# Kernel optimization log

Measured on AMD Instinct MI355X. Metric: run time of the kernel, lower is better.

## Reference

```python
import jax, jax.numpy as jnp
import numpy as np

B, T, C = 4, 1024, 768
N_HEAD = 12
HEAD_DIM = C // N_HEAD          # 64
WINDOW = 256                    # sliding window size
FIRE_WIDTH = 32
FIRE_INIT_L = 512.0
FIRE_EPS = 1e-6
ROPE_THETA = 10000.0


def setup_inputs() -> dict:
    key = jax.random.key(0)
    ks = jax.random.split(key, 8)
    s = 0.02
    return {
        "x": jax.random.normal(ks[0], (B, T, C), dtype=jnp.float32),
        "Wq": jax.random.normal(ks[1], (C, C), dtype=jnp.float32) * s,
        "Wk": jax.random.normal(ks[2], (C, C), dtype=jnp.float32) * s,
        "Wv": jax.random.normal(ks[3], (C, C), dtype=jnp.float32) * s,
        "Wproj": jax.random.normal(ks[4], (C, C), dtype=jnp.float32) * s,
        "fire_w1": jax.random.normal(ks[5], (1, FIRE_WIDTH), dtype=jnp.float32) * s,
        "fire_b1": jnp.zeros((FIRE_WIDTH,), dtype=jnp.float32),
        "fire_w2": jax.random.normal(ks[6], (FIRE_WIDTH, N_HEAD), dtype=jnp.float32) * s,
        "fire_b2": jnp.zeros((N_HEAD,), dtype=jnp.float32),
        "fire_c": jnp.asarray(0.1, dtype=jnp.float32),
        "fire_Lmult": jnp.asarray(1.0, dtype=jnp.float32),
        "iter_num": 1000,
    }


def _rope(t):
    # t: [B, H, T, D]; half-split rotary embedding
    d = t.shape[-1]
    pos = jnp.arange(t.shape[2], dtype=t.dtype)
    inv_freq = 1.0 / (ROPE_THETA ** (jnp.arange(0, d, 2, dtype=t.dtype) / d))
    ang = pos[:, None] * inv_freq[None, :]            # [T, D/2]
    cos, sin = jnp.cos(ang), jnp.sin(ang)
    t1, t2 = t[..., : d // 2], t[..., d // 2 :]
    return jnp.concatenate([t1 * cos - t2 * sin, t1 * sin + t2 * cos], axis=-1)


def _fire_bias(w1, b1, w2, b2, c, Lmult, Tlen, dtype):
    # FIRE: psi(i-j)/psi(max(i, L)) -> tiny MLP -> per-head bias [H, T, T]
    pos = jnp.arange(Tlen, dtype=dtype)
    rel = pos[:, None] - pos[None, :]                 # [T, T]
    thresh = jnp.abs(Lmult * FIRE_INIT_L)
    pos_norm = jnp.maximum(pos, thresh)
    rel_log = jnp.log(jnp.abs(c * rel) + 1.0)
    norm_log = jnp.log(jnp.abs(c * pos_norm) + 1.0) + FIRE_EPS
    z = (rel_log / norm_log[:, None])[..., None]      # [T, T, 1]
    h = jax.nn.relu(z @ w1 + b1)                      # [T, T, W]
    bias = h @ w2 + b2                                # [T, T, H]
    return jnp.transpose(bias, (2, 0, 1))             # [H, T, T]


def reference(x, Wq, Wk, Wv, Wproj, fire_w1, fire_b1, fire_w2, fire_b2,
              fire_c, fire_Lmult, iter_num):
    Bx, Tx, Cx = x.shape
    q = (x @ Wq).reshape(Bx, Tx, N_HEAD, HEAD_DIM).transpose(0, 2, 1, 3)
    k = (x @ Wk).reshape(Bx, Tx, N_HEAD, HEAD_DIM).transpose(0, 2, 1, 3)
    v = (x @ Wv).reshape(Bx, Tx, N_HEAD, HEAD_DIM).transpose(0, 2, 1, 3)
    q, k = _rope(q), _rope(k)

    att = jnp.einsum("bhqd,bhkd->bhqk", q, k) / jnp.sqrt(
        jnp.asarray(HEAD_DIM, x.dtype))
    att = att + _fire_bias(fire_w1, fire_b1, fire_w2, fire_b2,
                           fire_c, fire_Lmult, Tx, x.dtype)[None]

    # sliding-window causal mask: 0 <= q_idx - kv_idx <= WINDOW
    idx = jnp.arange(Tx)
    rel = idx[:, None] - idx[None, :]
    allowed = (rel >= 0) & (rel <= WINDOW)            # [T, T]
    att = jnp.where(allowed[None, None], att, jnp.asarray(-jnp.inf, att.dtype))
    att = jax.nn.softmax(att, axis=-1)

    y = jnp.einsum("bhqk,bhkd->bhqd", att, v)
    y = y.transpose(0, 2, 1, 3).reshape(Bx, Tx, Cx)
    return y @ Wproj
```

## Files before the change

### kernel.cpp

```cpp
#include <hip/hip_runtime.h>

typedef unsigned short u16;
typedef __attribute__((ext_vector_type(8))) short bf16x8;
typedef __attribute__((ext_vector_type(4))) float f32x4;

#define NB 4
#define NT 1024
#define NC 768
#define NH 12
#define HD 64

__device__ __forceinline__ u16 f2bf(float f) {
  union { float f; unsigned u; } v; v.f = f;
  unsigned r = v.u + 0x7FFFu + ((v.u >> 16) & 1u);
  return (u16)(r >> 16);
}
__device__ __forceinline__ float bf2f(u16 h) {
  union { unsigned u; float f; } v; v.u = ((unsigned)h) << 16;
  return v.f;
}

__device__ __forceinline__ void gld16(const u16* g, u16* l) {
  __builtin_amdgcn_global_load_lds((const __attribute__((address_space(1))) void*)g,
                                   (__attribute__((address_space(3))) void*)l, 16, 0, 0);
}

__global__ __launch_bounds__(256) void prep_k(const float* __restrict__ x,
                                              const float* __restrict__ Wq,
                                              const float* __restrict__ Wk,
                                              const float* __restrict__ Wv,
                                              const float* __restrict__ Wp,
                                              const float* __restrict__ w1,
                                              const float* __restrict__ b1,
                                              const float* __restrict__ w2,
                                              const float* __restrict__ b2,
                                              const float* __restrict__ cP,
                                              const float* __restrict__ LmP,
                                              u16* __restrict__ xb,
                                              u16* __restrict__ Wt,
                                              u16* __restrict__ Wtp,
                                              u16* __restrict__ ebias) {
  __shared__ u16 tile[64][65];
  const int bid = blockIdx.x;
  const int tid = threadIdx.x;
  if (bid < 1536) {
    const int base = bid * 2048 + tid * 8;
    const f32x4* xv = (const f32x4*)(x + base);
    f32x4 v0 = xv[0], v1 = xv[1];
    bf16x8 o;
#pragma unroll
    for (int j = 0; j < 4; ++j) {
      o[j] = (short)f2bf(v0[j]);
      o[4 + j] = (short)f2bf(v1[j]);
    }
    *(bf16x8*)(xb + base) = o;
  } else if (bid < 2112) {
    int idx = bid - 1536;
    int z = idx / 144, rem = idx - z * 144;
    int k0 = (rem / 12) * 64, n0 = (rem % 12) * 64;
    const float* src = (z == 0) ? Wq : (z == 1) ? Wk : (z == 2) ? Wv : Wp;
    const int c = tid & 63, r4 = tid >> 6;
#pragma unroll
    for (int p = 0; p < 16; ++p) {
      int kk = p * 4 + r4;
      tile[kk][c] = f2bf(src[(size_t)(k0 + kk) * NC + n0 + c]);
    }
    __syncthreads();
    u16* dst = (z < 3) ? (Wt + (size_t)z * NC * NC) : Wtp;
#pragma unroll
    for (int p = 0; p < 16; ++p) {
      int nn = p * 4 + r4;
      dst[(size_t)(n0 + nn) * NC + k0 + c] = tile[c][nn];
    }
  } else {
    int q = bid - 2112;
    float c = cP[0], Lm = LmP[0];
    float thresh = fabsf(Lm * 512.0f);
    float pn = fmaxf((float)q, thresh);
    float inv_nl = 1.0f / (logf(fabsf(c * pn) + 1.0f) + 1e-6f);
    for (int idx = tid; idx < 384; idx += 256) {
      int rel = idx - 64;
      float out[NH];
      if (rel >= 0 && rel <= 256) {
        float z = logf(fabsf(c * (float)rel) + 1.0f) * inv_nl;
        float acc[NH];
#pragma unroll
        for (int hh = 0; hh < NH; ++hh) acc[hh] = b2[hh];
#pragma unroll
        for (int j = 0; j < 32; ++j) {
          float hj = fmaxf(z * w1[j] + b1[j], 0.0f);
#pragma unroll
          for (int hh = 0; hh < NH; ++hh) acc[hh] += hj * w2[j * NH + hh];
        }
#pragma unroll
        for (int hh = 0; hh < NH; ++hh) out[hh] = __expf(acc[hh]);
      } else {
#pragma unroll
        for (int hh = 0; hh < NH; ++hh) out[hh] = 0.0f;
      }
#pragma unroll
      for (int hh = 0; hh < NH; ++hh)
        ebias[((size_t)hh * NT + q) * 384 + idx] = f2bf(out[hh]);
    }
  }
}

__global__ __launch_bounds__(256, 3) void gemm_qkv_rope(const u16* __restrict__ A,
                                                        const u16* __restrict__ Bt,
                                                        u16* __restrict__ Qp,
                                                        u16* __restrict__ Kp,
                                                        u16* __restrict__ Vp) {
  constexpr int K = NC;
  __shared__ __align__(16) u16 smem[9472];
  u16* As = smem;
  u16* Bs = smem + 4096;
  const int tid = threadIdx.x;
  const int wid = tid >> 6, lane = tid & 63;
  const int wr = wid >> 1, wc = wid & 1;
  const int m0 = blockIdx.x * 128, n0 = blockIdx.y * 128;
  const int lr = lane & 15, lg = lane >> 4, lk = lg << 3;
  const int srow = wid * 16 + (lane >> 2);
  const int scol = (lane & 3) * 8;
  f32x4 acc[4][4] = {};
  const u16* Ag = A + (size_t)(m0 + srow) * K + scol;
  const u16* Bg = Bt + (size_t)(n0 + srow) * K + scol;
  u16* Al = &As[(wid * 16) * 32];
  u16* Bl = &Bs[(wid * 16) * 32];

  for (int k0 = 0; k0 < K; k0 += 32) {
    gld16(Ag + k0, Al);
    gld16(Ag + (size_t)64 * K + k0, Al + 64 * 32);
    gld16(Bg + k0, Bl);
    gld16(Bg + (size_t)64 * K + k0, Bl + 64 * 32);
    __syncthreads();
    bf16x8 af[4], bfv[4];
#pragma unroll
    for (int i = 0; i < 4; ++i)
      af[i] = *(const bf16x8*)&As[(wr * 64 + i * 16 + lr) * 32 + lk];
#pragma unroll
    for (int j = 0; j < 4; ++j)
      bfv[j] = *(const bf16x8*)&Bs[(wc * 64 + j * 16 + lr) * 32 + lk];
#pragma unroll
    for (int i = 0; i < 4; ++i)
#pragma unroll
      for (int j = 0; j < 4; ++j)
        acc[i][j] = __builtin_amdgcn_mfma_f32_16x16x32_bf16(af[i], bfv[j], acc[i][j], 0, 0, 0);
    __syncthreads();
  }

  const int rbase = lg * 4;
  const int base_col = n0 + wc * 64;
  const int part = base_col / 768;
  const int h = (base_col % 768) >> 6;
  const int b = m0 >> 10;
  const int bh = b * NH + h;
  const int tbase = (m0 & 1023) + wr * 64;

  if (part < 2) {
    u16* dst = (part == 0 ? Qp : Kp) + ((size_t)bh << 16);
    const float inv0 = __expf(-(float)lr * 0.28782313662425f);
    const float inv1 = __expf(-(float)(lr + 16) * 0.28782313662425f);
#pragma unroll
    for (int i = 0; i < 4; ++i)
#pragma unroll
      for (int rr = 0; rr < 4; ++rr) {
        const int tl = tbase + i * 16 + rbase + rr;
        float s0, c0, s1, c1;
        __sincosf((float)tl * inv0, &s0, &c0);
        __sincosf((float)tl * inv1, &s1, &c1);
        const float a0 = acc[i][0][rr], a1 = acc[i][1][rr];
        const float a2 = acc[i][2][rr], a3 = acc[i][3][rr];
        const size_t ro = (size_t)tl * HD;
        dst[ro + lr]      = f2bf(a0 * c0 - a2 * s0);
        dst[ro + 16 + lr] = f2bf(a1 * c1 - a3 * s1);
        dst[ro + 32 + lr] = f2bf(a0 * s0 + a2 * c0);
        dst[ro + 48 + lr] = f2bf(a1 * s1 + a3 * c1);
      }
  } else {
    u16* dst = Vp + ((size_t)bh << 16);
    u16* vb = smem + wid * 64 * 37;
#pragma unroll
    for (int hf = 0; hf < 2; ++hf) {
#pragma unroll
      for (int i = 0; i < 4; ++i)
#pragma unroll
        for (int rr = 0; rr < 4; ++rr) {
          const int row = i * 16 + rbase + rr;
          vb[row * 37 + lr]      = f2bf(acc[i][2 * hf][rr]);
          vb[row * 37 + 16 + lr] = f2bf(acc[i][2 * hf + 1][rr]);
        }
      asm volatile("s_waitcnt lgkmcnt(0)" ::: "memory");
#pragma unroll
      for (int p = 0; p < 32; ++p) {
        const int d = hf * 32 + p;
        dst[(size_t)d * NT + tbase + lane] = vb[lane * 37 + p];
      }
    }
  }
}

template <bool F32OUT, int WR, int WC, int AI, int BJ>
__global__ __launch_bounds__(256, 4) void gemm_lds(const u16* __restrict__ A,
                                                   const u16* __restrict__ Bt,
                                                   void* __restrict__ Cv,
                                                   int M, int N, int K) {
  constexpr int BM = WR * AI * 16;
  constexpr int BN = WC * BJ * 16;
  __shared__ u16 As[BM * 32];
  __shared__ u16 Bs[BN * 32];
  const int tid = threadIdx.x;
  const int wid = tid >> 6, lane = tid & 63;
  const int wr = wid / WC, wc = wid % WC;
  const int m0 = blockIdx.x * BM, n0 = blockIdx.y * BN;
  const int lr = lane & 15, lk = (lane >> 4) << 3;
  const int srow = wid * 16 + (lane >> 2);
  const int scol = (lane & 3) * 8;
  f32x4 acc[AI][BJ] = {};
  const u16* Ag = A + (size_t)(m0 + srow) * K + scol;
  const u16* Bg = Bt + (size_t)(n0 + srow) * K + scol;
  u16* Al = &As[(wid * 16) * 32];
  u16* Bl = &Bs[(wid * 16) * 32];

  for (int k0 = 0; k0 < K; k0 += 32) {
#pragma unroll
    for (int ia = 0; ia < BM / 64; ++ia)
      gld16(Ag + (size_t)(ia * 64) * K + k0, Al + ia * 64 * 32);
#pragma unroll
    for (int ib = 0; ib < BN / 64; ++ib)
      gld16(Bg + (size_t)(ib * 64) * K + k0, Bl + ib * 64 * 32);
    __syncthreads();
    bf16x8 af[AI], bfv[BJ];
#pragma unroll
    for (int i = 0; i < AI; ++i)
      af[i] = *(const bf16x8*)&As[(wr * AI * 16 + i * 16 + lr) * 32 + lk];
#pragma unroll
    for (int j = 0; j < BJ; ++j)
      bfv[j] = *(const bf16x8*)&Bs[(wc * BJ * 16 + j * 16 + lr) * 32 + lk];
#pragma unroll
    for (int i = 0; i < AI; ++i)
#pragma unroll
      for (int j = 0; j < BJ; ++j)
        acc[i][j] = __builtin_amdgcn_mfma_f32_16x16x32_bf16(af[i], bfv[j], acc[i][j], 0, 0, 0);
    __syncthreads();
  }
  const int rbase = (lane >> 4) * 4;
#pragma unroll
  for (int i = 0; i < AI; ++i)
#pragma unroll
    for (int j = 0; j < BJ; ++j)
#pragma unroll
      for (int r = 0; r < 4; ++r) {
        size_t row = m0 + wr * AI * 16 + i * 16 + rbase + r;
        size_t col = n0 + wc * BJ * 16 + j * 16 + lr;
        if (F32OUT)
          ((float*)Cv)[row * N + col] = acc[i][j][r];
        else
          ((u16*)Cv)[row * N + col] = f2bf(acc[i][j][r]);
      }
}

__global__ __launch_bounds__(256, 3) void attn_k(const u16* __restrict__ Q,
                                                 const u16* __restrict__ K,
                                                 const u16* __restrict__ Vt,
                                                 const u16* __restrict__ ebias,
                                                 u16* __restrict__ Y) {
  __shared__ __align__(16) u16 Ks[2][64][64];
  __shared__ __align__(16) u16 Vs[2][64][64];
  __shared__ __align__(16) u16 plds[4][16][72];
  const int bid = blockIdx.x;
  const int xcd = bid & 7, j = bid >> 3;
  const int qb = j & 15, t6 = j >> 4;
  const int yslot = xcd * 6 + t6;
  const int b = yslot & 3, h = yslot >> 2;
  const int bh = b * NH + h;
  const int Q0 = qb << 6;
  const int tid = threadIdx.x, wid = tid >> 6, lane = tid & 63;
  const int q0 = Q0 + wid * 16;
  const int lr = lane & 15, lg = lane >> 4, lk = lg << 3;
  const u16* Qb = Q + ((size_t)bh << 16);
  const u16* Kb = K + ((size_t)bh << 16);
  const u16* Vb = Vt + ((size_t)bh << 16);
  const u16* ebh = ebias + (size_t)h * NT * 384;

  bf16x8 aq0 = *(const bf16x8*)(Qb + (q0 + lr) * HD + lk);
  bf16x8 aq1 = *(const bf16x8*)(Qb + (q0 + lr) * HD + 32 + lk);
  bf16x8 ones;
#pragma unroll
  for (int i = 0; i < 8; ++i) ones[i] = (short)0x3F80;
  f32x4 yacc[4] = {};
  f32x4 lsum = {};
  u16(*pl)[72] = plds[wid];

  int cstart = Q0 - 256;
  if (cstart < 0) cstart = 0;
  const int n = ((Q0 + 64) - cstart) >> 6;

  const int srow = lane >> 3;
  const int sseg = (lane & 7) ^ srow;
  auto STAGE = [&](int buf, int c) {
#pragma unroll
    for (int i = 0; i < 2; ++i) {
      const int rb = (i * 4 + wid) * 8;
      gld16(Kb + (size_t)(c + rb + srow) * HD + sseg * 8, &Ks[buf][rb][0]);
      gld16(Vb + (size_t)(rb + srow) * NT + c + sseg * 8, &Vs[buf][rb][0]);
    }
  };

  STAGE(0, cstart);
  __syncthreads();

  int c = cstart;
  for (int ci = 0; ci < n; ++ci, c += 64) {
    const int cur = ci & 1;
    if (ci + 1 < n) STAGE(cur ^ 1, c + 64);
    float eb[4][4];
#pragma unroll
    for (int kk = 0; kk < 4; ++kk) {
      const int kcol = c + kk * 16 + lr;
#pragma unroll
      for (int r = 0; r < 4; ++r) {
        int qrow = q0 + lg * 4 + r;
        int idx = qrow - kcol + 64;
        idx = idx < 0 ? 0 : (idx > 383 ? 383 : idx);
        eb[kk][r] = bf2f(ebh[(size_t)qrow * 384 + idx]);
      }
    }
    const int rsw = (lr & 7) << 4;
#pragma unroll
    for (int kk = 0; kk < 4; ++kk) {
      const char* krow = (const char*)&Ks[cur][kk * 16 + lr][0];
      bf16x8 bk0 = *(const bf16x8*)(krow + ((lg * 16) ^ rsw));
      bf16x8 bk1 = *(const bf16x8*)(krow + ((lg * 16 + 64) ^ rsw));
      f32x4 t = {};
      t = __builtin_amdgcn_mfma_f32_16x16x32_bf16(aq0, bk0, t, 0, 0, 0);
      t = __builtin_amdgcn_mfma_f32_16x16x32_bf16(aq1, bk1, t, 0, 0, 0);
#pragma unroll
      for (int r = 0; r < 4; ++r) {
        float p = __expf(t[r] * 0.125f) * eb[kk][r];
        pl[lg * 4 + r][kk * 16 + lr] = f2bf(p);
      }
    }
    asm volatile("s_waitcnt lgkmcnt(0)" ::: "memory");
    bf16x8 ap0 = *(const bf16x8*)&pl[lr][lk];
    bf16x8 ap1 = *(const bf16x8*)&pl[lr][32 + lk];
    lsum = __builtin_amdgcn_mfma_f32_16x16x32_bf16(ap0, ones, lsum, 0, 0, 0);
    lsum = __builtin_amdgcn_mfma_f32_16x16x32_bf16(ap1, ones, lsum, 0, 0, 0);
#pragma unroll
    for (int dt = 0; dt < 4; ++dt) {
      const char* vrow = (const char*)&Vs[cur][dt * 16 + lr][0];
      bf16x8 bv0 = *(const bf16x8*)(vrow + ((lg * 16) ^ rsw));
      bf16x8 bv1 = *(const bf16x8*)(vrow + ((lg * 16 + 64) ^ rsw));
      yacc[dt] = __builtin_amdgcn_mfma_f32_16x16x32_bf16(ap0, bv0, yacc[dt], 0, 0, 0);
      yacc[dt] = __builtin_amdgcn_mfma_f32_16x16x32_bf16(ap1, bv1, yacc[dt], 0, 0, 0);
    }
    __syncthreads();
  }

  float linv[4];
#pragma unroll
  for (int r = 0; r < 4; ++r) linv[r] = 1.0f / lsum[r];
#pragma unroll
  for (int dt = 0; dt < 4; ++dt)
#pragma unroll
    for (int r = 0; r < 4; ++r) {
      int qrow = q0 + lg * 4 + r;
      int d = dt * 16 + lr;
      Y[(size_t)(b * NT + qrow) * NC + h * HD + d] = f2bf(yacc[dt][r] * linv[r]);
    }
}

static constexpr size_t OFF_XB = 0;
static constexpr size_t OFF_WT = OFF_XB + 6291456;
static constexpr size_t OFF_WTP = OFF_WT + 3538944;
static constexpr size_t OFF_Q = OFF_WTP + 1179648;
static constexpr size_t OFF_K = OFF_Q + 6291456;
static constexpr size_t OFF_VT = OFF_K + 6291456;
static constexpr size_t OFF_BIAS = OFF_VT + 6291456;
static constexpr size_t OFF_Y = OFF_BIAS + 9437184;

extern "C" void kernel_launch(void* const* d_in, const int* in_sizes, int n_in,
                              void* d_out, int out_size, void* d_ws, size_t ws_size,
                              hipStream_t stream) {
  const float* x = (const float*)d_in[0];
  const float* Wq = (const float*)d_in[1];
  const float* Wk = (const float*)d_in[2];
  const float* Wv = (const float*)d_in[3];
  const float* Wp = (const float*)d_in[4];
  const float* fw1 = (const float*)d_in[5];
  const float* fb1 = (const float*)d_in[6];
  const float* fw2 = (const float*)d_in[7];
  const float* fb2 = (const float*)d_in[8];
  const float* fc = (const float*)d_in[9];
  const float* fLm = (const float*)d_in[10];

  char* ws = (char*)d_ws;
  u16* xb = (u16*)(ws + OFF_XB);
  u16* Wt = (u16*)(ws + OFF_WT);
  u16* Wtp = (u16*)(ws + OFF_WTP);
  u16* Qb = (u16*)(ws + OFF_Q);
  u16* Kb = (u16*)(ws + OFF_K);
  u16* Vtb = (u16*)(ws + OFF_VT);
  u16* ebiasb = (u16*)(ws + OFF_BIAS);
  u16* Yb = (u16*)(ws + OFF_Y);

  prep_k<<<3136, 256, 0, stream>>>(x, Wq, Wk, Wv, Wp, fw1, fb1, fw2, fb2, fc, fLm,
                                   xb, Wt, Wtp, ebiasb);
  gemm_qkv_rope<<<dim3(32, 18), 256, 0, stream>>>(xb, Wt, Qb, Kb, Vtb);
  attn_k<<<768, 256, 0, stream>>>(Qb, Kb, Vtb, ebiasb, Yb);
  gemm_lds<true, 2, 2, 4, 2><<<dim3(32, 12), 256, 0, stream>>>(Yb, Wtp, d_out, 4096, 768, 768);
}
```

Baseline: 75.26 us.

## Move FIRE bias into QKV GEMM launch, swizzle tiles, prefetch bias in attention

The FIRE bias table computation moves from the prep kernel into extra blocks of the QKV GEMM launch, which becomes a 1D grid of 1600 blocks. The 576 GEMM blocks get a remapped tile order, which may help L2 locality. The bias work then runs alongside GEMM compute rather than in the memory-bound prep pass. Separately, the attention kernel prefetches the next chunk's bias values into registers while computing the current chunk, hiding global load latency. This costs extra registers, and the bias blocks can compete with GEMM blocks for compute units.

```diff
diff --git a/kernel.cpp b/kernel.cpp
--- a/kernel.cpp
+++ b/kernel.cpp
@@ -30,16 +30,9 @@
                                               const float* __restrict__ Wk,
                                               const float* __restrict__ Wv,
                                               const float* __restrict__ Wp,
-                                              const float* __restrict__ w1,
-                                              const float* __restrict__ b1,
-                                              const float* __restrict__ w2,
-                                              const float* __restrict__ b2,
-                                              const float* __restrict__ cP,
-                                              const float* __restrict__ LmP,
                                               u16* __restrict__ xb,
                                               u16* __restrict__ Wt,
-                                              u16* __restrict__ Wtp,
-                                              u16* __restrict__ ebias) {
+                                              u16* __restrict__ Wtp) {
   __shared__ u16 tile[64][65];
   const int bid = blockIdx.x;
   const int tid = threadIdx.x;
@@ -54,7 +47,7 @@
       o[4 + j] = (short)f2bf(v1[j]);
     }
     *(bf16x8*)(xb + base) = o;
-  } else if (bid < 2112) {
+  } else {
     int idx = bid - 1536;
     int z = idx / 144, rem = idx - z * 144;
     int k0 = (rem / 12) * 64, n0 = (rem % 12) * 64;
@@ -72,8 +65,28 @@
       int nn = p * 4 + r4;
       dst[(size_t)(n0 + nn) * NC + k0 + c] = tile[c][nn];
     }
-  } else {
-    int q = bid - 2112;
+  }
+}
+
+__global__ __launch_bounds__(256, 3) void gemm_qkv_rope(const u16* __restrict__ A,
+                                                        const u16* __restrict__ Bt,
+                                                        const float* __restrict__ w1,
+                                                        const float* __restrict__ b1,
+                                                        const float* __restrict__ w2,
+                                                        const float* __restrict__ b2,
+                                                        const float* __restrict__ cP,
+                                                        const float* __restrict__ LmP,
+                                                        u16* __restrict__ Qp,
+                                                        u16* __restrict__ Kp,
+                                                        u16* __restrict__ Vp,
+                                                        u16* __restrict__ ebias) {
+  constexpr int K = NC;
+  __shared__ __align__(16) u16 smem[9472];
+  const int bid0 = blockIdx.x;
+  const int tid = threadIdx.x;
+
+  if (bid0 >= 576) {
+    int q = bid0 - 576;
     float c = cP[0], Lm = LmP[0];
     float thresh = fabsf(Lm * 512.0f);
     float pn = fmaxf((float)q, thresh);
@@ -102,22 +115,15 @@
       for (int hh = 0; hh < NH; ++hh)
         ebias[((size_t)hh * NT + q) * 384 + idx] = f2bf(out[hh]);
     }
-  }
-}
-
-__global__ __launch_bounds__(256, 3) void gemm_qkv_rope(const u16* __restrict__ A,
-                                                        const u16* __restrict__ Bt,
-                                                        u16* __restrict__ Qp,
-                                                        u16* __restrict__ Kp,
-                                                        u16* __restrict__ Vp) {
-  constexpr int K = NC;
-  __shared__ __align__(16) u16 smem[9472];
+    return;
+  }
+
   u16* As = smem;
   u16* Bs = smem + 4096;
-  const int tid = threadIdx.x;
+  const int lin = (bid0 & 7) * 72 + (bid0 >> 3);
+  const int m0 = (lin & 31) * 128, n0 = (lin >> 5) * 128;
   const int wid = tid >> 6, lane = tid & 63;
   const int wr = wid >> 1, wc = wid & 1;
-  const int m0 = blockIdx.x * 128, n0 = blockIdx.y * 128;
   const int lr = lane & 15, lg = lane >> 4, lk = lg << 3;
   const int srow = wid * 16 + (lane >> 2);
   const int scol = (lane & 3) * 8;
@@ -305,15 +311,7 @@
       gld16(Vb + (size_t)(rb + srow) * NT + c + sseg * 8, &Vs[buf][rb][0]);
     }
   };
-
-  STAGE(0, cstart);
-  __syncthreads();
-
-  int c = cstart;
-  for (int ci = 0; ci < n; ++ci, c += 64) {
-    const int cur = ci & 1;
-    if (ci + 1 < n) STAGE(cur ^ 1, c + 64);
-    float eb[4][4];
+  auto LOADEB = [&](float (&e)[4][4], int c) {
 #pragma unroll
     for (int kk = 0; kk < 4; ++kk) {
       const int kcol = c + kk * 16 + lr;
@@ -322,9 +320,23 @@
         int qrow = q0 + lg * 4 + r;
         int idx = qrow - kcol + 64;
         idx = idx < 0 ? 0 : (idx > 383 ? 383 : idx);
-        eb[kk][r] = bf2f(ebh[(size_t)qrow * 384 + idx]);
-      }
-    }
+        e[kk][r] = bf2f(ebh[(size_t)qrow * 384 + idx]);
+      }
+    }
+  };
+
+  STAGE(0, cstart);
+  float ebc[4][4];
+  LOADEB(ebc, cstart);
+  __syncthreads();
+
+  int c = cstart;
+  for (int ci = 0; ci < n; ++ci, c += 64) {
+    const int cur = ci & 1;
+    const bool more = (ci + 1 < n);
+    if (more) STAGE(cur ^ 1, c + 64);
+    float ebn[4][4];
+    if (more) LOADEB(ebn, c + 64);
     const int rsw = (lr & 7) << 4;
 #pragma unroll
     for (int kk = 0; kk < 4; ++kk) {
@@ -336,7 +348,7 @@
       t = __builtin_amdgcn_mfma_f32_16x16x32_bf16(aq1, bk1, t, 0, 0, 0);
 #pragma unroll
       for (int r = 0; r < 4; ++r) {
-        float p = __expf(t[r] * 0.125f) * eb[kk][r];
+        float p = __expf(t[r] * 0.125f) * ebc[kk][r];
         pl[lg * 4 + r][kk * 16 + lr] = f2bf(p);
       }
     }
@@ -352,6 +364,12 @@
       bf16x8 bv1 = *(const bf16x8*)(vrow + ((lg * 16 + 64) ^ rsw));
       yacc[dt] = __builtin_amdgcn_mfma_f32_16x16x32_bf16(ap0, bv0, yacc[dt], 0, 0, 0);
       yacc[dt] = __builtin_amdgcn_mfma_f32_16x16x32_bf16(ap1, bv1, yacc[dt], 0, 0, 0);
+    }
+    if (more) {
+#pragma unroll
+      for (int kk = 0; kk < 4; ++kk)
+#pragma unroll
+        for (int r = 0; r < 4; ++r) ebc[kk][r] = ebn[kk][r];
     }
     __syncthreads();
   }
@@ -403,9 +421,9 @@
   u16* ebiasb = (u16*)(ws + OFF_BIAS);
   u16* Yb = (u16*)(ws + OFF_Y);
 
-  prep_k<<<3136, 256, 0, stream>>>(x, Wq, Wk, Wv, Wp, fw1, fb1, fw2, fb2, fc, fLm,
-                                   xb, Wt, Wtp, ebiasb);
-  gemm_qkv_rope<<<dim3(32, 18), 256, 0, stream>>>(xb, Wt, Qb, Kb, Vtb);
+  prep_k<<<2112, 256, 0, stream>>>(x, Wq, Wk, Wv, Wp, xb, Wt, Wtp);
+  gemm_qkv_rope<<<1600, 256, 0, stream>>>(xb, Wt, fw1, fb1, fw2, fb2, fc, fLm,
+                                          Qb, Kb, Vtb, ebiasb);
   attn_k<<<768, 256, 0, stream>>>(Qb, Kb, Vtb, ebiasb, Yb);
   gemm_lds<true, 2, 2, 4, 2><<<dim3(32, 12), 256, 0, stream>>>(Yb, Wtp, d_out, 4096, 768, 768);
 }
```

New measurement: 68.27 us (median of 3 runs). 9.3% less time.
